# Performance work log

Hardware: AMD Instinct MI355X
Metric: run time of the kernel (lower is better)

## Reference

```python
import jax, jax.numpy as jnp
import numpy as np

HID, QK_NOPE, QK_ROPE, Q_LR, KV_LR, H, V_DIM = 2048, 128, 64, 768, 512, 16, 128
QK_HEAD = QK_NOPE + QK_ROPE
THETA = 10000.0
EPS = 1e-5


def _layernorm(x, g, b):
    mu = jnp.mean(x, axis=-1, keepdims=True)
    var = jnp.mean(jnp.square(x - mu), axis=-1, keepdims=True)
    return (x - mu) * jax.lax.rsqrt(var + EPS) * g + b


def _rotate_half(x):
    x1, x2 = jnp.split(x, 2, axis=-1)
    return jnp.concatenate([-x2, x1], axis=-1)


def setup_inputs() -> dict:
    key = jax.random.key(0)
    ks = jax.random.split(key, 6)
    s = 0.02
    return {
        "hidden_state": jax.random.normal(ks[0], (2, 4096, HID), dtype=jnp.float32),
        "w_qa": jax.random.normal(ks[1], (Q_LR, HID), dtype=jnp.float32) * s,
        "b_qa": jnp.zeros((Q_LR,), jnp.float32),
        "g_qa_ln": jnp.ones((Q_LR,), jnp.float32),
        "b_qa_ln": jnp.zeros((Q_LR,), jnp.float32),
        "w_qb": jax.random.normal(ks[2], (H * QK_HEAD, Q_LR), dtype=jnp.float32) * s,
        "b_qb": jnp.zeros((H * QK_HEAD,), jnp.float32),
        "w_kva": jax.random.normal(ks[3], (KV_LR + QK_ROPE, HID), dtype=jnp.float32) * s,
        "b_kva": jnp.zeros((KV_LR + QK_ROPE,), jnp.float32),
        "g_kva_ln": jnp.ones((KV_LR,), jnp.float32),
        "b_kva_ln": jnp.zeros((KV_LR,), jnp.float32),
        "w_kvb": jax.random.normal(ks[4], (H * (QK_NOPE + V_DIM), KV_LR), dtype=jnp.float32) * s,
        "b_kvb": jnp.zeros((H * (QK_NOPE + V_DIM),), jnp.float32),
    }


def reference(hidden_state, w_qa, b_qa, g_qa_ln, b_qa_ln, w_qb, b_qb,
              w_kva, b_kva, g_kva_ln, b_kva_ln, w_kvb, b_kvb):
    B, S, _ = hidden_state.shape
    # ----- Q path: low-rank down-proj -> LN -> up-proj -----
    q_c = hidden_state @ w_qa.T + b_qa                      # [B,S,Q_LR]
    q_c = _layernorm(q_c, g_qa_ln, b_qa_ln)
    q = (q_c @ w_qb.T + b_qb).reshape(B, S, H, QK_HEAD).transpose(0, 2, 1, 3)  # [B,H,S,QK_HEAD]
    q_nope, q_rope = q[..., :QK_NOPE], q[..., QK_NOPE:]
    # ----- KV path -----
    kv_c = hidden_state @ w_kva.T + b_kva                   # [B,S,KV_LR+ROPE]
    kv_lr, k_rope = kv_c[..., :KV_LR], kv_c[..., KV_LR:]
    kv_lr = _layernorm(kv_lr, g_kva_ln, b_kva_ln)
    kv = (kv_lr @ w_kvb.T + b_kvb).reshape(B, S, H, QK_NOPE + V_DIM).transpose(0, 2, 1, 3)
    k_nope, v = kv[..., :QK_NOPE], kv[..., QK_NOPE:]
    # ----- RoPE on the rope slice only -----
    inv_freq = 1.0 / THETA ** (jnp.arange(0, QK_ROPE, 2, dtype=jnp.float32) / QK_ROPE)
    freq = jnp.arange(S, dtype=jnp.float32)[:, None] * inv_freq[None, :]   # [S, ROPE/2]
    cos = jnp.concatenate([jnp.cos(freq), jnp.cos(freq)], axis=-1)[None, None]  # [1,1,S,ROPE]
    sin = jnp.concatenate([jnp.sin(freq), jnp.sin(freq)], axis=-1)[None, None]
    k_rope = k_rope[:, None]                                # [B,1,S,ROPE]
    q_rot = q_rope * cos + _rotate_half(q_rope) * sin       # [B,H,S,ROPE]
    k_rot = k_rope * cos + _rotate_half(k_rope) * sin       # [B,1,S,ROPE]
    k_rot = jnp.broadcast_to(k_rot, (B, H, S, QK_ROPE))
    q_full = jnp.concatenate([q_nope, q_rot], axis=-1)      # [B,H,S,QK_HEAD]
    k_full = jnp.concatenate([k_nope, k_rot], axis=-1)      # [B,H,S,QK_HEAD]
    # original forward stops after building q,k,v; return them concatenated
    return jnp.concatenate([q_full, k_full, v], axis=-1)    # [B,H,S,2*QK_HEAD+V_DIM]
```

## Files before the change

kernel.cpp:

```cpp
#include <hip/hip_runtime.h>

typedef unsigned short u16;
typedef __bf16 bf16x8 __attribute__((ext_vector_type(8)));
typedef float f32x4 __attribute__((ext_vector_type(4)));


__device__ __forceinline__ u16 f2bf(float f) {
  unsigned u = __float_as_uint(f);
  u += 0x7fffu + ((u >> 16) & 1u);
  return (u16)(u >> 16);
}

__device__ __forceinline__ ushort4 f2bf4(float4 v) {
  return make_ushort4(f2bf(v.x), f2bf(v.y), f2bf(v.z), f2bf(v.w));
}

__device__ __forceinline__ void load_lds16(const void* g, void* l) {
  __builtin_amdgcn_global_load_lds(
      (const __attribute__((address_space(1))) void*)g,
      (__attribute__((address_space(3))) void*)l, 16, 0, 0);
}

__device__ __forceinline__ void conv_seg(const float* __restrict__ s,
                                         u16* __restrict__ d, int n4,
                                         int g, int stride) {
  const float4* s4 = (const float4*)s;
  ushort4* d4 = (ushort4*)d;
  for (int i = g; i < n4; i += stride) {
    float4 v = s4[i];
    d4[i] = make_ushort4(f2bf(v.x), f2bf(v.y), f2bf(v.z), f2bf(v.w));
  }
}


__global__ __launch_bounds__(256) void prep(
    const float* __restrict__ hid, const float* __restrict__ wqa,
    const float* __restrict__ wkva, const float* __restrict__ wqb,
    const float* __restrict__ wkvb, const float* __restrict__ bqa,
    const float* __restrict__ bkva, u16* __restrict__ hid_b,
    u16* __restrict__ wab_b, u16* __restrict__ wqb_b,
    u16* __restrict__ wkvb_b, float* __restrict__ bias_ab,
    float* __restrict__ cosT, float* __restrict__ sinT) {
  int g = blockIdx.x * 256 + threadIdx.x;
  int stride = gridDim.x * 256;
  conv_seg(hid, hid_b, 4194304, g, stride);
  conv_seg(wqa, wab_b, 393216, g, stride);
  conv_seg(wkva, wab_b + 768 * 2048, 294912, g, stride);
  conv_seg(wqb, wqb_b, 589824, g, stride);
  conv_seg(wkvb, wkvb_b, 524288, g, stride);
  if (g < 1344) bias_ab[g] = (g < 768) ? bqa[g] : bkva[g - 768];
  for (int idx = g; idx < 131072; idx += stride) {
    int s = idx >> 5, i = idx & 31;
    float inv = powf(10000.f, -(float)i / 32.f);
    float f = (float)s * inv;
    float sv, cv;
    sincosf(f, &sv, &cv);
    cosT[idx] = cv;
    sinT[idx] = sv;
  }
}


template <int WHICH>
__global__ __launch_bounds__(256, 2) void gemm_k(
    const u16* __restrict__ A0, const u16* __restrict__ B0,
    const float* __restrict__ bias0, float* __restrict__ C0,
    const u16* __restrict__ qA, const u16* __restrict__ qB,
    const float* __restrict__ qb, const u16* __restrict__ kA,
    const u16* __restrict__ kB, const float* __restrict__ kb,
    float* __restrict__ out, const float* __restrict__ cosT,
    const float* __restrict__ sinT) {
  __shared__ __align__(16) u16 smem[2 * 128 * 64];
  u16* sA = smem;
  u16* sB = smem + 128 * 64;
  const int tid = threadIdx.x;
  const int lane = tid & 63;
  const int wave = tid >> 6;
  const int wm = (wave >> 1) * 64;
  const int wn = (wave & 1) * 64;
  const int lane15 = lane & 15;
  const int quad = lane >> 4;
  const int mTile = blockIdx.x * 128;

  const u16* A;
  const u16* B;
  const float* bias;
  int K, nTile, mode;
  if (WHICH == 0) {
    A = A0; B = B0; bias = bias0; K = 2048; nTile = blockIdx.y * 128; mode = 0;
  } else if (blockIdx.y < 24) {
    A = qA; B = qB; bias = qb; K = 768; nTile = blockIdx.y * 128; mode = 1;
  } else {
    A = kA; B = kB; bias = kb; K = 512; nTile = (blockIdx.y - 24) * 128;
    mode = 2;
  }

  f32x4 acc[4][4] = {};

  const int nStages = K >> 6;
  for (int ks = 0; ks < nStages; ++ks) {
    const int k0 = ks << 6;
    if (ks) __syncthreads();
#pragma unroll
    for (int i = 0; i < 4; ++i) {
      int nu = i * 256 + tid;
      int rr = nu >> 3, u = nu & 7;
      int ul = u ^ (rr & 7);
      load_lds16(A + (size_t)(mTile + rr) * K + (k0 + ul * 8),
                 &sA[(i * 256 + (wave << 6)) * 8]);
    }
#pragma unroll
    for (int i = 0; i < 4; ++i) {
      int nu = i * 256 + tid;
      int rr = nu >> 3, u = nu & 7;
      int ul = u ^ (rr & 7);
      int brow = nTile + rr;
      if (WHICH == 0 && brow >= 1344) brow = 1343;
      load_lds16(B + (size_t)brow * K + (k0 + ul * 8),
                 &sB[(i * 256 + (wave << 6)) * 8]);
    }
    __syncthreads();
#pragma unroll
    for (int kk = 0; kk < 2; ++kk) {
      bf16x8 af[4], bfv[4];
#pragma unroll
      for (int mi = 0; mi < 4; ++mi) {
        int r = wm + mi * 16 + lane15;
        int u = (kk * 4 + quad) ^ (r & 7);
        af[mi] = *(const bf16x8*)&sA[(r * 8 + u) * 8];
      }
#pragma unroll
      for (int ni = 0; ni < 4; ++ni) {
        int r = wn + ni * 16 + lane15;
        int u = (kk * 4 + quad) ^ (r & 7);
        bfv[ni] = *(const bf16x8*)&sB[(r * 8 + u) * 8];
      }
#pragma unroll
      for (int mi = 0; mi < 4; ++mi)
#pragma unroll
        for (int ni = 0; ni < 4; ++ni)
          acc[mi][ni] = __builtin_amdgcn_mfma_f32_16x16x32_bf16(
              af[mi], bfv[ni], acc[mi][ni], 0, 0, 0);
    }
  }

  const int colW = nTile + wn;
  float bv[4];
#pragma unroll
  for (int ni = 0; ni < 4; ++ni) {
    int col = colW + ni * 16 + lane15;
    if (WHICH == 0)
      bv[ni] = (col < 1344) ? bias[col] : 0.f;
    else
      bv[ni] = bias[col];
  }

  int h = 0, ch0 = 0;
  if (mode == 1) {
    h = colW / 192;
    ch0 = colW % 192;
  } else if (mode == 2) {
    int jb = colW & 255;
    h = colW >> 8;
    ch0 = (jb < 128) ? (192 + jb) : (256 + jb);
  }
  const bool ropeTile = (mode == 1) && (ch0 == 128);

  __syncthreads();
  float* lw = (float*)smem + wave * (16 * 68);
  const int hi = lane15 >> 2, l3 = lane15 & 3;

#pragma unroll
  for (int mi = 0; mi < 4; ++mi) {
    f32x4 v[4];
#pragma unroll
    for (int ni = 0; ni < 4; ++ni)
#pragma unroll
      for (int rg = 0; rg < 4; ++rg) v[ni][rg] = acc[mi][ni][rg] + bv[ni];

    if (ropeTile) {
      int rowB = mTile + wm + mi * 16 + quad * 4;
#pragma unroll
      for (int rg = 0; rg < 4; ++rg) {
        int ss = (rowB + rg) & 4095;
#pragma unroll
        for (int ni = 0; ni < 2; ++ni) {
          int i = ni * 16 + lane15;
          float cv = cosT[ss * 32 + i], sv = sinT[ss * 32 + i];
          float x1 = v[ni][rg], x2 = v[ni + 2][rg];
          v[ni][rg] = x1 * cv - x2 * sv;
          v[ni + 2][rg] = x2 * cv + x1 * sv;
        }
      }
    }

    if (mi) asm volatile("s_waitcnt lgkmcnt(0)" ::: "memory");
#pragma unroll
    for (int ni = 0; ni < 4; ++ni) {
      int su = (4 * ni + hi) ^ quad;
#pragma unroll
      for (int rg = 0; rg < 4; ++rg)
        lw[68 * (quad * 4 + rg) + 4 * su + l3] = v[ni][rg];
    }
    asm volatile("s_waitcnt lgkmcnt(0)" ::: "memory");
#pragma unroll
    for (int j = 0; j < 4; ++j) {
      int rr = 4 * j + quad;
      int su = lane15 ^ j;
      float4 o = *(const float4*)&lw[68 * rr + 4 * su];
      int row = mTile + wm + mi * 16 + rr;
      if (mode == 0) {
        if (colW + 4 * lane15 < 1344)
          *(float4*)(C0 + (size_t)row * 1344 + colW + 4 * lane15) = o;
      } else {
        int bb = row >> 12, ss = row & 4095;
        size_t ob =
            ((size_t)((bb * 16 + h) * 4096 + ss)) * 512 + ch0 + 4 * lane15;
        *(float4*)(out + ob) = o;
      }
    }
  }
}


__global__ __launch_bounds__(256) void ln_rot(
    const float* __restrict__ qkvc, const float* __restrict__ g_q,
    const float* __restrict__ b_q, const float* __restrict__ g_kv,
    const float* __restrict__ b_kv, u16* __restrict__ q_ln,
    u16* __restrict__ kv_ln, const float* __restrict__ cosT,
    const float* __restrict__ sinT, float* __restrict__ out) {
  __shared__ float red[4][4];
  __shared__ __align__(16) float rot[64];
  const int tid = threadIdx.x;
  const int t = blockIdx.x;
  const int bb = t >> 12, ss = t & 4095;
  const float4* p4 = (const float4*)(qkvc + (size_t)t * 1344);

  float4 a = p4[tid];
  float4 b = make_float4(0.f, 0.f, 0.f, 0.f);
  if (tid < 80) b = p4[256 + tid];

  float sa = a.x + a.y + a.z + a.w;
  float sqa = a.x * a.x + a.y * a.y + a.z * a.z + a.w * a.w;
  float qs = 0.f, qq = 0.f, ks = 0.f, kq = 0.f;
  if (tid < 192) { qs = sa; qq = sqa; } else { ks = sa; kq = sqa; }
  if (tid < 64) {
    ks += b.x + b.y + b.z + b.w;
    kq += b.x * b.x + b.y * b.y + b.z * b.z + b.w * b.w;
  }
#pragma unroll
  for (int off = 32; off > 0; off >>= 1) {
    qs += __shfl_down(qs, off, 64);
    qq += __shfl_down(qq, off, 64);
    ks += __shfl_down(ks, off, 64);
    kq += __shfl_down(kq, off, 64);
  }
  const int lane = tid & 63, wave = tid >> 6;
  if (lane == 0) {
    red[wave][0] = qs; red[wave][1] = qq;
    red[wave][2] = ks; red[wave][3] = kq;
  }
  __syncthreads();
  qs = red[0][0] + red[1][0] + red[2][0] + red[3][0];
  qq = red[0][1] + red[1][1] + red[2][1] + red[3][1];
  ks = red[0][2] + red[1][2] + red[2][2] + red[3][2];
  kq = red[0][3] + red[1][3] + red[2][3] + red[3][3];
  const float muq = qs * (1.f / 768.f);
  const float invq = rsqrtf(qq * (1.f / 768.f) - muq * muq + 1e-5f);
  const float muk = ks * (1.f / 512.f);
  const float invk = rsqrtf(kq * (1.f / 512.f) - muk * muk + 1e-5f);

  if (tid < 192) {
    float4 g = ((const float4*)g_q)[tid];
    float4 be = ((const float4*)b_q)[tid];
    float4 o = make_float4((a.x - muq) * invq * g.x + be.x,
                           (a.y - muq) * invq * g.y + be.y,
                           (a.z - muq) * invq * g.z + be.z,
                           (a.w - muq) * invq * g.w + be.w);
    ((ushort4*)(q_ln + (size_t)t * 768))[tid] = f2bf4(o);
  } else {
    int j = tid - 192;
    float4 g = ((const float4*)g_kv)[j];
    float4 be = ((const float4*)b_kv)[j];
    float4 o = make_float4((a.x - muk) * invk * g.x + be.x,
                           (a.y - muk) * invk * g.y + be.y,
                           (a.z - muk) * invk * g.z + be.z,
                           (a.w - muk) * invk * g.w + be.w);
    ((ushort4*)(kv_ln + (size_t)t * 512))[j] = f2bf4(o);
  }
  if (tid < 64) {
    int j = 64 + tid;
    float4 g = ((const float4*)g_kv)[j];
    float4 be = ((const float4*)b_kv)[j];
    float4 o = make_float4((b.x - muk) * invk * g.x + be.x,
                           (b.y - muk) * invk * g.y + be.y,
                           (b.z - muk) * invk * g.z + be.z,
                           (b.w - muk) * invk * g.w + be.w);
    ((ushort4*)(kv_ln + (size_t)t * 512))[j] = f2bf4(o);
  }
  if (tid < 32) {
    const float* p = qkvc + (size_t)t * 1344;
    float k1 = p[1280 + tid], k2 = p[1312 + tid];
    float cv = cosT[ss * 32 + tid], sv = sinT[ss * 32 + tid];
    rot[tid] = k1 * cv - k2 * sv;
    rot[tid + 32] = k2 * cv + k1 * sv;
  }
  __syncthreads();
  {
    int hh = tid >> 4, c4 = tid & 15;
    float4 o = ((const float4*)rot)[c4];
    *(float4*)(out + ((size_t)((bb * 16 + hh) * 4096 + ss)) * 512 + 320 +
               4 * c4) = o;
  }
}


extern "C" void kernel_launch(void* const* d_in, const int* in_sizes, int n_in,
                              void* d_out, int out_size, void* d_ws,
                              size_t ws_size, hipStream_t stream) {
  const float* hidden = (const float*)d_in[0];
  const float* w_qa = (const float*)d_in[1];
  const float* b_qa = (const float*)d_in[2];
  const float* g_qa_ln = (const float*)d_in[3];
  const float* b_qa_ln = (const float*)d_in[4];
  const float* w_qb = (const float*)d_in[5];
  const float* b_qb = (const float*)d_in[6];
  const float* w_kva = (const float*)d_in[7];
  const float* b_kva = (const float*)d_in[8];
  const float* g_kva_ln = (const float*)d_in[9];
  const float* b_kva_ln = (const float*)d_in[10];
  const float* w_kvb = (const float*)d_in[11];
  const float* b_kvb = (const float*)d_in[12];
  float* out = (float*)d_out;

  char* ws = (char*)d_ws;
  u16* hid_bf = (u16*)ws;   ws += (size_t)16777216 * 2;
  u16* wab_bf = (u16*)ws;   ws += (size_t)1344 * 2048 * 2;
  u16* wqb_bf = (u16*)ws;   ws += (size_t)2359296 * 2;
  u16* wkvb_bf = (u16*)ws;  ws += (size_t)2097152 * 2;
  float* qkvc = (float*)ws; ws += (size_t)8192 * 1344 * 4;
  u16* q_ln = (u16*)ws;     ws += (size_t)6291456 * 2;
  u16* kv_ln = (u16*)ws;    ws += (size_t)4194304 * 2;
  float* cosT = (float*)ws; ws += (size_t)131072 * 4;
  float* sinT = (float*)ws; ws += (size_t)131072 * 4;
  float* bias_ab = (float*)ws; ws += (size_t)2048 * 4;

  prep<<<dim3(1024), dim3(256), 0, stream>>>(
      hidden, w_qa, w_kva, w_qb, w_kvb, b_qa, b_kva, hid_bf, wab_bf, wqb_bf,
      wkvb_bf, bias_ab, cosT, sinT);
  gemm_k<0><<<dim3(64, 11), dim3(256), 0, stream>>>(
      hid_bf, wab_bf, bias_ab, qkvc, nullptr, nullptr, nullptr, nullptr,
      nullptr, nullptr, nullptr, cosT, sinT);
  ln_rot<<<dim3(8192), dim3(256), 0, stream>>>(qkvc, g_qa_ln, b_qa_ln,
                                               g_kva_ln, b_kva_ln, q_ln, kv_ln,
                                               cosT, sinT, out);
  gemm_k<1><<<dim3(64, 56), dim3(256), 0, stream>>>(
      nullptr, nullptr, nullptr, nullptr, q_ln, wqb_bf, b_qb, kv_ln, wkvb_bf,
      b_kvb, out, cosT, sinT);
}
```

Before: 471.6 us.

## Split KV up-projection into dedicated 256x256-tile GEMM kernel

```diff
diff --git a/kernel.cpp b/kernel.cpp
--- a/kernel.cpp
+++ b/kernel.cpp
@@ -3,6 +3,14 @@
 typedef unsigned short u16;
 typedef __bf16 bf16x8 __attribute__((ext_vector_type(8)));
 typedef float f32x4 __attribute__((ext_vector_type(4)));
+
+#define FENCE() asm volatile("" ::: "memory")
+#define BARRIER()                      \
+  do {                                 \
+    FENCE();                           \
+    __builtin_amdgcn_s_barrier();      \
+    FENCE();                           \
+  } while (0)
 
 
 __device__ __forceinline__ u16 f2bf(float f) {
@@ -222,6 +230,137 @@
   }
 }
 
+__global__ __launch_bounds__(512, 2) void gemm256(
+    const u16* __restrict__ A, const u16* __restrict__ B,
+    const float* __restrict__ bias, float* __restrict__ out) {
+  __shared__ __align__(16) u16 smem[4 * 256 * 64];
+  const int tid = threadIdx.x;
+  const int lane = tid & 63;
+  const int wave = tid >> 6;
+  const int wm = (wave >> 2) * 128;
+  const int wn = (wave & 3) * 64;
+  const int lane15 = lane & 15;
+  const int quad = lane >> 4;
+  const int mTile = blockIdx.x * 256;
+  const int nTile = blockIdx.y * 256;
+
+  u16* const sA0 = smem;
+  u16* const sB0 = smem + 2 * 16384;
+
+#define STAGE8(kt, c)                                                         \
+  do {                                                                        \
+    u16* dA = sA0 + (c) * 16384;                                              \
+    u16* dB = sB0 + (c) * 16384;                                              \
+    _Pragma("unroll") for (int i = 0; i < 4; ++i) {                           \
+      int g = i * 512 + tid;                                                  \
+      int rr = g >> 3, ul = (g & 7) ^ (rr & 7);                               \
+      load_lds16(A + (size_t)(mTile + rr) * 512 + (kt) * 64 + ul * 8,         \
+                 dA + (i * 512 + (wave << 6)) * 8);                           \
+    }                                                                         \
+    _Pragma("unroll") for (int i = 0; i < 4; ++i) {                           \
+      int g = i * 512 + tid;                                                  \
+      int rr = g >> 3, ul = (g & 7) ^ (rr & 7);                               \
+      load_lds16(B + (size_t)(nTile + rr) * 512 + (kt) * 64 + ul * 8,         \
+                 dB + (i * 512 + (wave << 6)) * 8);                           \
+    }                                                                         \
+  } while (0)
+
+  f32x4 acc[8][4] = {};
+
+  STAGE8(0, 0);
+  for (int t = 0; t < 8; ++t) {
+    const int c = t & 1;
+    const u16* sAc = sA0 + c * 16384;
+    const u16* sBc = sB0 + c * 16384;
+    if (t < 7) {
+      STAGE8(t + 1, c ^ 1);
+      asm volatile("s_waitcnt vmcnt(8)" ::: "memory");
+    } else {
+      asm volatile("s_waitcnt vmcnt(0)" ::: "memory");
+    }
+    BARRIER();
+#pragma unroll
+    for (int ph = 0; ph < 4; ++ph) {
+      const int mh = ph >> 1, nh = ph & 1;
+      bf16x8 af[4][2], bfv[2][2];
+#pragma unroll
+      for (int mi = 0; mi < 4; ++mi) {
+        int r = wm + mh * 64 + mi * 16 + lane15;
+#pragma unroll
+        for (int kk = 0; kk < 2; ++kk) {
+          int u = (kk * 4 + quad) ^ (r & 7);
+          af[mi][kk] = *(const bf16x8*)&sAc[(r * 8 + u) * 8];
+        }
+      }
+#pragma unroll
+      for (int ni = 0; ni < 2; ++ni) {
+        int rb = wn + nh * 32 + ni * 16 + lane15;
+#pragma unroll
+        for (int kk = 0; kk < 2; ++kk) {
+          int u = (kk * 4 + quad) ^ (rb & 7);
+          bfv[ni][kk] = *(const bf16x8*)&sBc[(rb * 8 + u) * 8];
+        }
+      }
+      BARRIER();
+      __builtin_amdgcn_s_setprio(1);
+#pragma unroll
+      for (int mi = 0; mi < 4; ++mi)
+#pragma unroll
+        for (int ni = 0; ni < 2; ++ni)
+#pragma unroll
+          for (int kk = 0; kk < 2; ++kk)
+            acc[mh * 4 + mi][nh * 2 + ni] =
+                __builtin_amdgcn_mfma_f32_16x16x32_bf16(
+                    af[mi][kk], bfv[ni][kk], acc[mh * 4 + mi][nh * 2 + ni],
+                    0, 0, 0);
+      __builtin_amdgcn_s_setprio(0);
+      BARRIER();
+    }
+  }
+#undef STAGE8
+
+  const int colW = nTile + wn;
+  float bv[4];
+#pragma unroll
+  for (int ni = 0; ni < 4; ++ni) bv[ni] = bias[colW + ni * 16 + lane15];
+  const int h = colW >> 8;
+  const int jb = colW & 255;
+  const int ch0 = (jb < 128) ? (192 + jb) : (256 + jb);
+
+  float* lw = (float*)smem + wave * (16 * 68);
+  const int hi = lane15 >> 2, l3 = lane15 & 3;
+
+#pragma unroll
+  for (int mi = 0; mi < 8; ++mi) {
+    f32x4 v[4];
+#pragma unroll
+    for (int ni = 0; ni < 4; ++ni)
+#pragma unroll
+      for (int rg = 0; rg < 4; ++rg) v[ni][rg] = acc[mi][ni][rg] + bv[ni];
+
+    if (mi) asm volatile("s_waitcnt lgkmcnt(0)" ::: "memory");
+#pragma unroll
+    for (int ni = 0; ni < 4; ++ni) {
+      int su = (4 * ni + hi) ^ quad;
+#pragma unroll
+      for (int rg = 0; rg < 4; ++rg)
+        lw[68 * (quad * 4 + rg) + 4 * su + l3] = v[ni][rg];
+    }
+    asm volatile("s_waitcnt lgkmcnt(0)" ::: "memory");
+#pragma unroll
+    for (int j = 0; j < 4; ++j) {
+      int rr = 4 * j + quad;
+      int su = lane15 ^ j;
+      float4 o = *(const float4*)&lw[68 * rr + 4 * su];
+      int row = mTile + wm + mi * 16 + rr;
+      int bb = row >> 12, ss = row & 4095;
+      size_t ob =
+          ((size_t)((bb * 16 + h) * 4096 + ss)) * 512 + ch0 + 4 * lane15;
+      *(float4*)(out + ob) = o;
+    }
+  }
+}
+
 
 __global__ __launch_bounds__(256) void ln_rot(
     const float* __restrict__ qkvc, const float* __restrict__ g_q,
@@ -354,7 +493,8 @@
   ln_rot<<<dim3(8192), dim3(256), 0, stream>>>(qkvc, g_qa_ln, b_qa_ln,
                                                g_kva_ln, b_kva_ln, q_ln, kv_ln,
                                                cosT, sinT, out);
-  gemm_k<1><<<dim3(64, 56), dim3(256), 0, stream>>>(
-      nullptr, nullptr, nullptr, nullptr, q_ln, wqb_bf, b_qb, kv_ln, wkvb_bf,
-      b_kvb, out, cosT, sinT);
-}
+  gemm_k<1><<<dim3(64, 24), dim3(256), 0, stream>>>(
+      nullptr, nullptr, nullptr, nullptr, q_ln, wqb_bf, b_qb, nullptr, nullptr,
+      nullptr, out, cosT, sinT);
+  gemm256<<<dim3(32, 16), dim3(512), 0, stream>>>(kv_ln, wkvb_bf, b_kvb, out);
+}
```

Result: no change. 480.3 us (+1.8%).
